# Kernel tuning notes

Hardware: AMD Instinct MI355X
Metric: run time of the kernel (lower is better)

Reference implementation:

```python
import jax, jax.numpy as jnp
import numpy as np

B, T, N, DIM = 2, 4096, 4, 2048
EPS = 1e-6
ALPHA_INIT = 0.01


def setup_inputs() -> dict:
    key = jax.random.key(0)
    k1, k2, k3, k4 = jax.random.split(key, 4)
    x_stream = jax.random.normal(k1, (B, T, N, DIM), dtype=jnp.float32)
    rms_weight = jnp.ones((DIM,), dtype=jnp.float32)
    theta_pre = 0.02 * jax.random.normal(k2, (DIM,), dtype=jnp.float32)
    theta_post = 0.02 * jax.random.normal(k3, (DIM,), dtype=jnp.float32)
    theta_res = 0.02 * jax.random.normal(k4, (N, DIM), dtype=jnp.float32)
    return {
        "x_stream": x_stream,
        "rms_weight": rms_weight,
        "alpha_pre": jnp.float32(ALPHA_INIT),
        "alpha_post": jnp.float32(ALPHA_INIT),
        "alpha_res": jnp.float32(ALPHA_INIT),
        "theta_pre": theta_pre,
        "theta_post": theta_post,
        "theta_res": theta_res,
        "b_pre": jnp.full((N,), 1.0 / N, dtype=jnp.float32),
        "b_post": jnp.ones((N,), dtype=jnp.float32),
        "b_res": jnp.eye(N, dtype=jnp.float32),
    }


def _rms_norm(x, weight, eps):
    x = x.astype(jnp.float32)
    var = jnp.mean(x * x, axis=-1, keepdims=True)
    return x * jax.lax.rsqrt(var + eps) * weight


def reference(x_stream, rms_weight, alpha_pre, alpha_post, alpha_res,
              theta_pre, theta_post, theta_res, b_pre, b_post, b_res):
    # x_stream: [B,T,n,dim]
    x_tilde = _rms_norm(x_stream, rms_weight, EPS)            # [B,T,n,dim]
    hpre_dyn = jnp.einsum('c,btnc->btn', theta_pre, x_tilde)  # [B,T,n]
    hpost_dyn = jnp.einsum('c,btnc->btn', theta_post, x_tilde)
    H_pre = alpha_pre * jnp.tanh(hpre_dyn) + b_pre
    H_post = alpha_post * jnp.tanh(hpost_dyn) + b_post
    hres_dyn = jnp.einsum('ic,btnc->btin', theta_res, x_tilde)  # [B,T,n,n]
    H_res = alpha_res * jnp.tanh(hres_dyn) + b_res
    return (H_pre, H_post, H_res)
```

## Files before the change

kernel.cpp:

```cpp
#include <hip/hip_runtime.h>
#include <math.h>

#define DIM     2048
#define NROWS   32768
#define EPS_RMS 1e-6f
#define NTH     6
#define BLK     1024
#define GRIDN   1024

__device__ __forceinline__ float fast_tanh(float x) {
    return 1.0f - 2.0f / (__expf(2.0f * x) + 1.0f);
}

#define DOT4(t, a) ((t).x*(a).x + (t).y*(a).y + (t).z*(a).z + (t).w*(a).w)

#define ROR_ADD(v, CTRL)                                                      \
    do {                                                                      \
        int _iv = __float_as_int(v);                                          \
        int _r  = __builtin_amdgcn_update_dpp(_iv, _iv, (CTRL), 0xF, 0xF, false); \
        (v) += __int_as_float(_r);                                            \
    } while (0)

#define WAVE_SUM(v)                                                           \
    do {                                                                      \
        ROR_ADD(v, 0x121);                                     \
        ROR_ADD(v, 0x122);                                     \
        ROR_ADD(v, 0x124);                                     \
        ROR_ADD(v, 0x128);                                     \
        (v) += __shfl_xor((v), 16);                                           \
        (v) += __shfl_xor((v), 32);                                           \
    } while (0)

__global__ __launch_bounds__(BLK, 4) void hcmaps_kernel(
    const float* __restrict__ x,
    const float* __restrict__ w,
    const float* __restrict__ alpha_pre_p,
    const float* __restrict__ alpha_post_p,
    const float* __restrict__ alpha_res_p,
    const float* __restrict__ theta_pre,
    const float* __restrict__ theta_post,
    const float* __restrict__ theta_res,
    const float* __restrict__ b_pre,
    const float* __restrict__ b_post,
    const float* __restrict__ b_res,
    float* __restrict__ out)
{
    __shared__ float s_wt[NTH * DIM];

    const int tid  = threadIdx.x;
    const int lane = tid & 63;
    const int wid  = tid >> 6;
    const int gw   = blockIdx.x * 16 + wid;
    const int r0   = gw;
    const int r1   = gw + 16384;

    const float4* __restrict__ xf4 = (const float4*)x;

    float4 xa[4], xb[4];
    {
        const float4* ra = xf4 + (size_t)r0 * 512;
        const float4* rb = xf4 + (size_t)r1 * 512;
#pragma unroll
        for (int j = 0; j < 4; ++j) {
            xa[j] = ra[j * 64 + lane];
            xb[j] = rb[j * 64 + lane];
        }
    }

#pragma unroll
    for (int it = 0; it < 3; ++it) {
        const int q  = tid + it * BLK;
        const int v  = q >> 9;
        const int cf = q & 511;
        const float* tb = (v == 0) ? theta_pre
                        : (v == 1) ? theta_post
                                   : (theta_res + (v - 2) * DIM);
        const float4 wv = ((const float4*)w)[cf];
        const float4 t4 = ((const float4*)tb)[cf];
        ((float4*)s_wt)[q] =
            make_float4(wv.x * t4.x, wv.y * t4.y, wv.z * t4.z, wv.w * t4.w);
    }

    const float apre  = alpha_pre_p[0];
    const float apost = alpha_post_p[0];
    const float ares  = alpha_res_p[0];
    const int   n     = gw & 3;
    const int   s     = lane & 7;
    float bias = 0.f, alpha = 0.f;
    if (s < 6) {
        alpha = (s == 0) ? apre : (s == 1) ? apost : ares;
        bias  = (s == 0) ? b_pre[n]
              : (s == 1) ? b_post[n]
                         : b_res[(s - 2) * 4 + n];
    }

    __syncthreads();

    float ssa = 0.f, ssb = 0.f;
    float da0 = 0.f, da1 = 0.f, da2 = 0.f, da3 = 0.f, da4 = 0.f, da5 = 0.f;
    float db0 = 0.f, db1 = 0.f, db2 = 0.f, db3 = 0.f, db4 = 0.f, db5 = 0.f;

#pragma unroll
    for (int chunk = 0; chunk < 2; ++chunk) {
        if (chunk == 1) {
            const float4* ra = xf4 + (size_t)r0 * 512 + 256;
            const float4* rb = xf4 + (size_t)r1 * 512 + 256;
#pragma unroll
            for (int j = 0; j < 4; ++j) {
                xa[j] = ra[j * 64 + lane];
                xb[j] = rb[j * 64 + lane];
            }
        }
#pragma unroll
        for (int j = 0; j < 4; ++j) {
            const float4 a = xa[j];
            const float4 b = xb[j];
            const float* tb = s_wt + chunk * 1024 + j * 256 + lane * 4;
            ssa += DOT4(a, a);
            ssb += DOT4(b, b);
            float4 t;
            t = *(const float4*)(tb + 0 * DIM); da0 += DOT4(t, a); db0 += DOT4(t, b);
            t = *(const float4*)(tb + 1 * DIM); da1 += DOT4(t, a); db1 += DOT4(t, b);
            t = *(const float4*)(tb + 2 * DIM); da2 += DOT4(t, a); db2 += DOT4(t, b);
            t = *(const float4*)(tb + 3 * DIM); da3 += DOT4(t, a); db3 += DOT4(t, b);
            t = *(const float4*)(tb + 4 * DIM); da4 += DOT4(t, a); db4 += DOT4(t, b);
            t = *(const float4*)(tb + 5 * DIM); da5 += DOT4(t, a); db5 += DOT4(t, b);
        }
    }

    WAVE_SUM(ssa); WAVE_SUM(ssb);
    WAVE_SUM(da0); WAVE_SUM(da1); WAVE_SUM(da2);
    WAVE_SUM(da3); WAVE_SUM(da4); WAVE_SUM(da5);
    WAVE_SUM(db0); WAVE_SUM(db1); WAVE_SUM(db2);
    WAVE_SUM(db3); WAVE_SUM(db4); WAVE_SUM(db5);

    const bool rowB = lane >= 8;
    if (s < 6 && lane < 14) {
        const float ss = rowB ? ssb : ssa;
        const float c0 = rowB ? db0 : da0;
        const float c1 = rowB ? db1 : da1;
        const float c2 = rowB ? db2 : da2;
        const float c3 = rowB ? db3 : da3;
        const float c4 = rowB ? db4 : da4;
        const float c5 = rowB ? db5 : da5;
        const float dv = (s == 0) ? c0 : (s == 1) ? c1 : (s == 2) ? c2
                       : (s == 3) ? c3 : (s == 4) ? c4 : c5;
        const int   r  = rowB ? r1 : r0;
        const float rstd = rsqrtf(ss * (1.0f / DIM) + EPS_RMS);
        const float val  = alpha * fast_tanh(dv * rstd) + bias;
        int addr;
        if (s == 0)      addr = r;
        else if (s == 1) addr = NROWS + r;
        else             addr = 2 * NROWS + (r >> 2) * 16 + (s - 2) * 4 + n;
        out[addr] = val;
    }
}

extern "C" void kernel_launch(void* const* d_in, const int* in_sizes, int n_in,
                              void* d_out, int out_size, void* d_ws, size_t ws_size,
                              hipStream_t stream) {
    const float* x          = (const float*)d_in[0];
    const float* rms_weight = (const float*)d_in[1];
    const float* alpha_pre  = (const float*)d_in[2];
    const float* alpha_post = (const float*)d_in[3];
    const float* alpha_res  = (const float*)d_in[4];
    const float* theta_pre  = (const float*)d_in[5];
    const float* theta_post = (const float*)d_in[6];
    const float* theta_res  = (const float*)d_in[7];
    const float* b_pre      = (const float*)d_in[8];
    const float* b_post     = (const float*)d_in[9];
    const float* b_res      = (const float*)d_in[10];
    float* out = (float*)d_out;

    dim3 grid(GRIDN);
    dim3 block(BLK);
    hipLaunchKernelGGL(hcmaps_kernel, grid, block, 0, stream,
                       x, rms_weight, alpha_pre, alpha_post, alpha_res,
                       theta_pre, theta_post, theta_res,
                       b_pre, b_post, b_res, out);
}
```

Baseline: 46.29 us.

## Process four rows per wave with full-row prefetch of next row pair

Halves the grid so each wave handles two row pairs instead of one. It loads both halves of each row up front, then prefetches the second row pair into registers while the first pair is reduced and written. The aim is to overlap global loads with the reduction and to amortize the shared-memory weight setup over more rows. This costs much higher register pressure, with 64 float4 values live per thread, and fewer blocks in flight.

```diff
diff --git a/kernel.cpp b/kernel.cpp
--- a/kernel.cpp
+++ b/kernel.cpp
@@ -6,7 +6,7 @@
 #define EPS_RMS 1e-6f
 #define NTH     6
 #define BLK     1024
-#define GRIDN   1024
+#define GRIDN   512
 
 __device__ __forceinline__ float fast_tanh(float x) {
     return 1.0f - 2.0f / (__expf(2.0f * x) + 1.0f);
@@ -24,12 +24,14 @@
 #define WAVE_SUM(v)                                                           \
     do {                                                                      \
         ROR_ADD(v, 0x121);                                     \
+        ROR_AD2(v)                                                            \
+    } while (0)
+#define ROR_AD2(v)                                                            \
         ROR_ADD(v, 0x122);                                     \
         ROR_ADD(v, 0x124);                                     \
         ROR_ADD(v, 0x128);                                     \
         (v) += __shfl_xor((v), 16);                                           \
-        (v) += __shfl_xor((v), 32);                                           \
-    } while (0)
+        (v) += __shfl_xor((v), 32);
 
 __global__ __launch_bounds__(BLK, 4) void hcmaps_kernel(
     const float* __restrict__ x,
@@ -51,19 +53,19 @@
     const int lane = tid & 63;
     const int wid  = tid >> 6;
     const int gw   = blockIdx.x * 16 + wid;
-    const int r0   = gw;
-    const int r1   = gw + 16384;
 
     const float4* __restrict__ xf4 = (const float4*)x;
 
-    float4 xa[4], xb[4];
-    {
-        const float4* ra = xf4 + (size_t)r0 * 512;
-        const float4* rb = xf4 + (size_t)r1 * 512;
+    float4 xa0[4], xa1[4], xb0[4], xb1[4];
+    {
+        const float4* ra = xf4 + (size_t)gw * 512;
+        const float4* rb = xf4 + ((size_t)gw + 16384) * 512;
 #pragma unroll
         for (int j = 0; j < 4; ++j) {
-            xa[j] = ra[j * 64 + lane];
-            xb[j] = rb[j * 64 + lane];
+            xa0[j] = ra[j * 64 + lane];
+            xb0[j] = rb[j * 64 + lane];
+            xa1[j] = ra[256 + j * 64 + lane];
+            xb1[j] = rb[256 + j * 64 + lane];
         }
     }
 
@@ -101,30 +103,41 @@
     float db0 = 0.f, db1 = 0.f, db2 = 0.f, db3 = 0.f, db4 = 0.f, db5 = 0.f;
 
 #pragma unroll
-    for (int chunk = 0; chunk < 2; ++chunk) {
-        if (chunk == 1) {
-            const float4* ra = xf4 + (size_t)r0 * 512 + 256;
-            const float4* rb = xf4 + (size_t)r1 * 512 + 256;
-#pragma unroll
-            for (int j = 0; j < 4; ++j) {
-                xa[j] = ra[j * 64 + lane];
-                xb[j] = rb[j * 64 + lane];
-            }
-        }
+    for (int j = 0; j < 4; ++j) {
+        const float4 a = xa0[j], b = xb0[j];
+        const float* tb = s_wt + j * 256 + lane * 4;
+        ssa += DOT4(a, a); ssb += DOT4(b, b);
+        float4 t;
+        t = *(const float4*)(tb + 0 * DIM); da0 += DOT4(t, a); db0 += DOT4(t, b);
+        t = *(const float4*)(tb + 1 * DIM); da1 += DOT4(t, a); db1 += DOT4(t, b);
+        t = *(const float4*)(tb + 2 * DIM); da2 += DOT4(t, a); db2 += DOT4(t, b);
+        t = *(const float4*)(tb + 3 * DIM); da3 += DOT4(t, a); db3 += DOT4(t, b);
+        t = *(const float4*)(tb + 4 * DIM); da4 += DOT4(t, a); db4 += DOT4(t, b);
+        t = *(const float4*)(tb + 5 * DIM); da5 += DOT4(t, a); db5 += DOT4(t, b);
+    }
+#pragma unroll
+    for (int j = 0; j < 4; ++j) {
+        const float4 a = xa1[j], b = xb1[j];
+        const float* tb = s_wt + 1024 + j * 256 + lane * 4;
+        ssa += DOT4(a, a); ssb += DOT4(b, b);
+        float4 t;
+        t = *(const float4*)(tb + 0 * DIM); da0 += DOT4(t, a); db0 += DOT4(t, b);
+        t = *(const float4*)(tb + 1 * DIM); da1 += DOT4(t, a); db1 += DOT4(t, b);
+        t = *(const float4*)(tb + 2 * DIM); da2 += DOT4(t, a); db2 += DOT4(t, b);
+        t = *(const float4*)(tb + 3 * DIM); da3 += DOT4(t, a); db3 += DOT4(t, b);
+        t = *(const float4*)(tb + 4 * DIM); da4 += DOT4(t, a); db4 += DOT4(t, b);
+        t = *(const float4*)(tb + 5 * DIM); da5 += DOT4(t, a); db5 += DOT4(t, b);
+    }
+
+    {
+        const float4* ra = xf4 + ((size_t)gw + 8192) * 512;
+        const float4* rb = xf4 + ((size_t)gw + 24576) * 512;
 #pragma unroll
         for (int j = 0; j < 4; ++j) {
-            const float4 a = xa[j];
-            const float4 b = xb[j];
-            const float* tb = s_wt + chunk * 1024 + j * 256 + lane * 4;
-            ssa += DOT4(a, a);
-            ssb += DOT4(b, b);
-            float4 t;
-            t = *(const float4*)(tb + 0 * DIM); da0 += DOT4(t, a); db0 += DOT4(t, b);
-            t = *(const float4*)(tb + 1 * DIM); da1 += DOT4(t, a); db1 += DOT4(t, b);
-            t = *(const float4*)(tb + 2 * DIM); da2 += DOT4(t, a); db2 += DOT4(t, b);
-            t = *(const float4*)(tb + 3 * DIM); da3 += DOT4(t, a); db3 += DOT4(t, b);
-            t = *(const float4*)(tb + 4 * DIM); da4 += DOT4(t, a); db4 += DOT4(t, b);
-            t = *(const float4*)(tb + 5 * DIM); da5 += DOT4(t, a); db5 += DOT4(t, b);
+            xa0[j] = ra[j * 64 + lane];
+            xb0[j] = rb[j * 64 + lane];
+            xa1[j] = ra[256 + j * 64 + lane];
+            xb1[j] = rb[256 + j * 64 + lane];
         }
     }
 
@@ -133,26 +146,86 @@
     WAVE_SUM(da3); WAVE_SUM(da4); WAVE_SUM(da5);
     WAVE_SUM(db0); WAVE_SUM(db1); WAVE_SUM(db2);
     WAVE_SUM(db3); WAVE_SUM(db4); WAVE_SUM(db5);
-
-    const bool rowB = lane >= 8;
-    if (s < 6 && lane < 14) {
-        const float ss = rowB ? ssb : ssa;
-        const float c0 = rowB ? db0 : da0;
-        const float c1 = rowB ? db1 : da1;
-        const float c2 = rowB ? db2 : da2;
-        const float c3 = rowB ? db3 : da3;
-        const float c4 = rowB ? db4 : da4;
-        const float c5 = rowB ? db5 : da5;
-        const float dv = (s == 0) ? c0 : (s == 1) ? c1 : (s == 2) ? c2
-                       : (s == 3) ? c3 : (s == 4) ? c4 : c5;
-        const int   r  = rowB ? r1 : r0;
-        const float rstd = rsqrtf(ss * (1.0f / DIM) + EPS_RMS);
-        const float val  = alpha * fast_tanh(dv * rstd) + bias;
-        int addr;
-        if (s == 0)      addr = r;
-        else if (s == 1) addr = NROWS + r;
-        else             addr = 2 * NROWS + (r >> 2) * 16 + (s - 2) * 4 + n;
-        out[addr] = val;
+    {
+        const bool rowB = lane >= 8;
+        if (s < 6 && lane < 14) {
+            const float ss = rowB ? ssb : ssa;
+            const float c0 = rowB ? db0 : da0;
+            const float c1 = rowB ? db1 : da1;
+            const float c2 = rowB ? db2 : da2;
+            const float c3 = rowB ? db3 : da3;
+            const float c4 = rowB ? db4 : da4;
+            const float c5 = rowB ? db5 : da5;
+            const float dv = (s == 0) ? c0 : (s == 1) ? c1 : (s == 2) ? c2
+                           : (s == 3) ? c3 : (s == 4) ? c4 : c5;
+            const int   r  = rowB ? (gw + 16384) : gw;
+            const float rstd = rsqrtf(ss * (1.0f / DIM) + EPS_RMS);
+            const float val  = alpha * fast_tanh(dv * rstd) + bias;
+            int addr;
+            if (s == 0)      addr = r;
+            else if (s == 1) addr = NROWS + r;
+            else             addr = 2 * NROWS + (r >> 2) * 16 + (s - 2) * 4 + n;
+            out[addr] = val;
+        }
+    }
+
+    ssa = 0.f; ssb = 0.f;
+    da0 = 0.f; da1 = 0.f; da2 = 0.f; da3 = 0.f; da4 = 0.f; da5 = 0.f;
+    db0 = 0.f; db1 = 0.f; db2 = 0.f; db3 = 0.f; db4 = 0.f; db5 = 0.f;
+
+#pragma unroll
+    for (int j = 0; j < 4; ++j) {
+        const float4 a = xa0[j], b = xb0[j];
+        const float* tb = s_wt + j * 256 + lane * 4;
+        ssa += DOT4(a, a); ssb += DOT4(b, b);
+        float4 t;
+        t = *(const float4*)(tb + 0 * DIM); da0 += DOT4(t, a); db0 += DOT4(t, b);
+        t = *(const float4*)(tb + 1 * DIM); da1 += DOT4(t, a); db1 += DOT4(t, b);
+        t = *(const float4*)(tb + 2 * DIM); da2 += DOT4(t, a); db2 += DOT4(t, b);
+        t = *(const float4*)(tb + 3 * DIM); da3 += DOT4(t, a); db3 += DOT4(t, b);
+        t = *(const float4*)(tb + 4 * DIM); da4 += DOT4(t, a); db4 += DOT4(t, b);
+        t = *(const float4*)(tb + 5 * DIM); da5 += DOT4(t, a); db5 += DOT4(t, b);
+    }
+#pragma unroll
+    for (int j = 0; j < 4; ++j) {
+        const float4 a = xa1[j], b = xb1[j];
+        const float* tb = s_wt + 1024 + j * 256 + lane * 4;
+        ssa += DOT4(a, a); ssb += DOT4(b, b);
+        float4 t;
+        t = *(const float4*)(tb + 0 * DIM); da0 += DOT4(t, a); db0 += DOT4(t, b);
+        t = *(const float4*)(tb + 1 * DIM); da1 += DOT4(t, a); db1 += DOT4(t, b);
+        t = *(const float4*)(tb + 2 * DIM); da2 += DOT4(t, a); db2 += DOT4(t, b);
+        t = *(const float4*)(tb + 3 * DIM); da3 += DOT4(t, a); db3 += DOT4(t, b);
+        t = *(const float4*)(tb + 4 * DIM); da4 += DOT4(t, a); db4 += DOT4(t, b);
+        t = *(const float4*)(tb + 5 * DIM); da5 += DOT4(t, a); db5 += DOT4(t, b);
+    }
+
+    WAVE_SUM(ssa); WAVE_SUM(ssb);
+    WAVE_SUM(da0); WAVE_SUM(da1); WAVE_SUM(da2);
+    WAVE_SUM(da3); WAVE_SUM(da4); WAVE_SUM(da5);
+    WAVE_SUM(db0); WAVE_SUM(db1); WAVE_SUM(db2);
+    WAVE_SUM(db3); WAVE_SUM(db4); WAVE_SUM(db5);
+    {
+        const bool rowB = lane >= 8;
+        if (s < 6 && lane < 14) {
+            const float ss = rowB ? ssb : ssa;
+            const float c0 = rowB ? db0 : da0;
+            const float c1 = rowB ? db1 : da1;
+            const float c2 = rowB ? db2 : da2;
+            const float c3 = rowB ? db3 : da3;
+            const float c4 = rowB ? db4 : da4;
+            const float c5 = rowB ? db5 : da5;
+            const float dv = (s == 0) ? c0 : (s == 1) ? c1 : (s == 2) ? c2
+                           : (s == 3) ? c3 : (s == 4) ? c4 : c5;
+            const int   r  = rowB ? (gw + 24576) : (gw + 8192);
+            const float rstd = rsqrtf(ss * (1.0f / DIM) + EPS_RMS);
+            const float val  = alpha * fast_tanh(dv * rstd) + bias;
+            int addr;
+            if (s == 0)      addr = r;
+            else if (s == 1) addr = NROWS + r;
+            else             addr = 2 * NROWS + (r >> 2) * 16 + (s - 2) * 4 + n;
+            out[addr] = val;
+        }
     }
 }
 
```

After: 71.33 us. 54.1% more time.
